# Optimization experiments

Measured on AMD Instinct MI355X. Metric: run time of the kernel, lower is better.

The kernel has to match this reference:

```python
import jax, jax.numpy as jnp
import numpy as np
import math

B, BERT_DIM, COND, INUM, RNN, TDIFF, SAMPLE_T, TEMB, TMAX = 16384, 768, 64, 10, 128, 200, 50, 64, 64


def _schedule():
    steps = TDIFF + 1
    x = np.linspace(0, TDIFF, steps) / TDIFF
    ab = np.cos((x + 0.008) / 1.008 * np.pi / 2) ** 2
    ab = ab / ab[0]
    betas = np.minimum(1.0 - ab[1:] / ab[:-1], 0.9999)
    alphas = 1.0 - betas
    alpha_bar = np.cumprod(alphas)
    stride = max(TDIFF // SAMPLE_T, 1)
    ts = np.array(list(range(TDIFF - 1, -1, -stride)), dtype=np.int64)  # 50 steps: 199..3
    abt = alpha_bar[ts]
    abp = np.where(ts > 0, alpha_bar[np.maximum(ts - 1, 0)], 1.0)
    beta = betas[ts]
    coef1 = np.sqrt(abp) * beta / (1 - abt)
    coef2 = np.sqrt(alphas[ts]) * (1 - abp) / (1 - abt)
    var = (1 - abp) / (1 - abt) * beta
    sqrtvar = np.where(ts > 0, np.sqrt(var), 0.0)
    return ts, coef1.astype(np.float32), coef2.astype(np.float32), sqrtvar.astype(np.float32)


def _sinusoidal_emb(ts, dim):
    half = dim // 2
    freq = jnp.exp(-math.log(10000.0) * jnp.arange(half, dtype=jnp.float32) / (half - 1))
    emb = ts.astype(jnp.float32)[:, None] * freq[None, :]
    return jnp.concatenate([jnp.sin(emb), jnp.cos(emb)], axis=-1)


def setup_inputs() -> dict:
    key = jax.random.key(0)
    ks = jax.random.split(key, 40)
    i = iter(range(40))

    def lin(kout, kin):  # torch Linear layout (out, in), Kaiming-ish scale
        kw, kb = jax.random.split(ks[next(i)])
        return (jax.random.normal(kw, (kout, kin), jnp.float32) / np.sqrt(kin),
                jax.random.normal(kb, (kout,), jnp.float32) * 0.01)

    inp = {}
    inp['bert_emb'] = jax.random.normal(ks[next(i)], (B, BERT_DIM), jnp.float32)
    # sorted, positive event times (padded)
    raw = jax.random.uniform(ks[next(i)], (B, TMAX), jnp.float32)
    inp['times'] = jnp.cumsum(raw * 0.05, axis=1)
    inp['init_noise'] = jax.random.normal(ks[next(i)], (B, INUM), jnp.float32)
    inp['step_noise'] = jax.random.normal(ks[next(i)], (SAMPLE_T, B, INUM), jnp.float32)

    inp['bp_w'], inp['bp_b'] = lin(COND, BERT_DIM)
    inp['ln_g'] = jnp.ones((COND,), jnp.float32)
    inp['ln_b'] = jnp.zeros((COND,), jnp.float32)
    inp['tp_w1'], inp['tp_b1'] = lin(TEMB * 2, TEMB)
    inp['tp_w2'], inp['tp_b2'] = lin(TEMB, TEMB * 2)
    den_in = INUM + COND + TEMB  # 138
    inp['dn_w1'], inp['dn_b1'] = lin(256, den_in)
    inp['dn_w2'], inp['dn_b2'] = lin(256, 256)
    inp['dn_w3'], inp['dn_b3'] = lin(INUM, 256)
    inp['sf_w1'], inp['sf_b1'] = lin(INUM * 2, INUM)
    inp['sf_w2'], inp['sf_b2'] = lin(INUM * 2, INUM * 2)
    inp['sf_w3'], inp['sf_b3'] = lin(INUM, INUM * 2)
    inp['h0_w'], inp['h0_b'] = lin(RNN, COND + INUM)
    inp['gru_wi'], inp['gru_bi'] = lin(3 * RNN, 1)
    inp['gru_wh'], inp['gru_bh'] = lin(3 * RNN, RNN)
    inp['hd_w'], inp['hd_b'] = lin(2, RNN)
    return inp


def _forward(bert_emb, times, init_noise, step_noise,
             bp_w, bp_b, ln_g, ln_b,
             tp_w1, tp_b1, tp_w2, tp_b2,
             dn_w1, dn_b1, dn_w2, dn_b2, dn_w3, dn_b3,
             sf_w1, sf_b1, sf_w2, sf_b2, sf_w3, sf_b3,
             h0_w, h0_b, gru_wi, gru_wh, gru_bi, gru_bh, hd_w, hd_b):
    # --- bert_proj: Linear + LayerNorm (dropout = identity at eval) ---
    c = bert_emb @ bp_w.T + bp_b
    mu = jnp.mean(c, axis=-1, keepdims=True)
    var = jnp.var(c, axis=-1, keepdims=True)
    cond = (c - mu) * jax.lax.rsqrt(var + 1e-5) * ln_g + ln_b  # (B, COND)

    # --- DDPM ancestral sampling over interval features ---
    ts_np, c1_np, c2_np, sv_np = _schedule()
    ts = jnp.asarray(ts_np)
    c1, c2, sv = jnp.asarray(c1_np), jnp.asarray(c2_np), jnp.asarray(sv_np)
    temb = _sinusoidal_emb(ts, TEMB)                     # (S, 64)
    te = jax.nn.silu(temb @ tp_w1.T + tp_b1) @ tp_w2.T + tp_b2  # (S, 64)

    def ddpm_step(x, args):
        te_s, c1_s, c2_s, sv_s, nz = args
        inp = jnp.concatenate([x, cond, jnp.broadcast_to(te_s, (x.shape[0], TEMB))], axis=-1)
        h = jax.nn.silu(inp @ dn_w1.T + dn_b1)
        h = jax.nn.silu(h @ dn_w2.T + dn_b2)
        x0p = h @ dn_w3.T + dn_b3
        x_new = c1_s * x0p + c2_s * x + sv_s * nz
        return x_new, None

    x0, _ = jax.lax.scan(ddpm_step, init_noise, (te, c1, c2, sv, step_noise))  # (B, INUM)

    # --- GRU decoder (teacher-forced forward_train) ---
    seq_emb = jax.nn.relu(x0 @ sf_w1.T + sf_b1)
    seq_emb = jax.nn.relu(seq_emb @ sf_w2.T + sf_b2)
    seq_emb = seq_emb @ sf_w3.T + sf_b3                  # (B, INUM)
    h0 = jnp.tanh(jnp.concatenate([cond, seq_emb], axis=-1) @ h0_w.T + h0_b)  # (B, RNN)

    gt_times = jnp.concatenate([jnp.zeros((times.shape[0], 1), times.dtype), times], axis=1)
    gt_delta = gt_times[:, 1:] - gt_times[:, :-1]        # (B, T)
    # x_in at step 0 is zeros, then gt_delta[:, i-1]
    x_in_seq = jnp.concatenate([jnp.zeros((1, times.shape[0], 1), times.dtype),
                                gt_delta.T[:, :, None]], axis=0)  # (T+1, B, 1)

    def gru_step(h, x_in):
        gi = x_in @ gru_wi.T + gru_bi                    # (B, 3*RNN)
        gh = h @ gru_wh.T + gru_bh
        gi_r, gi_z, gi_n = jnp.split(gi, 3, axis=-1)
        gh_r, gh_z, gh_n = jnp.split(gh, 3, axis=-1)
        r = jax.nn.sigmoid(gi_r + gh_r)
        z = jax.nn.sigmoid(gi_z + gh_z)
        n = jnp.tanh(gi_n + r * gh_n)
        h_new = (1.0 - z) * n + z * h
        out = h_new @ hd_w.T + hd_b                      # (B, 2)
        return h_new, out

    _, outs = jax.lax.scan(gru_step, h0, x_in_seq)       # (T+1, B, 2)
    pred_delta = outs[:, :, 0].T                         # (B, T+1)
    stop_logits = outs[:, :, 1].T
    return x0, pred_delta, stop_logits


def reference(bert_emb, times, init_noise, step_noise,
              bp_w, bp_b, ln_g, ln_b,
              tp_w1, tp_b1, tp_w2, tp_b2,
              dn_w1, dn_b1, dn_w2, dn_b2, dn_w3, dn_b3,
              sf_w1, sf_b1, sf_w2, sf_b2, sf_w3, sf_b3,
              h0_w, h0_b, gru_wi, gru_wh, gru_bi, gru_bh, hd_w, hd_b):
    return _forward(bert_emb, times, init_noise, step_noise,
                    bp_w, bp_b, ln_g, ln_b,
                    tp_w1, tp_b1, tp_w2, tp_b2,
                    dn_w1, dn_b1, dn_w2, dn_b2, dn_w3, dn_b3,
                    sf_w1, sf_b1, sf_w2, sf_b2, sf_w3, sf_b3,
                    h0_w, h0_b, gru_wi, gru_wh, gru_bi, gru_bh, hd_w, hd_b)
```

## Files before the change

### kernel.cpp

```cpp
#include <hip/hip_runtime.h>
#include <math.h>

typedef float f4 __attribute__((ext_vector_type(4)));
typedef float f32x4 __attribute__((ext_vector_type(4)));
typedef _Float16 f16;
typedef _Float16 f16x8 __attribute__((ext_vector_type(8)));

#define NB 16384
#define BERT_DIM 768
#define CONDD 64
#define INUMD 10
#define RNND 128
#define TDIFFN 200
#define SAMPLE_TN 50
#define TEMBD 64
#define TMAXN 64

struct Sched { float c1[SAMPLE_TN], c2[SAMPLE_TN], sv[SAMPLE_TN], ts[SAMPLE_TN]; };

__device__ __forceinline__ float fsig(float v)  { return __builtin_amdgcn_rcpf(1.f + __expf(-v)); }
__device__ __forceinline__ float ftanh(float v) { return 1.f - 2.f * __builtin_amdgcn_rcpf(1.f + __expf(2.f * v)); }
__device__ __forceinline__ float fsilu(float v) { return v * fsig(v); }

__global__ __launch_bounds__(256) void pack_kernel(
    const float* __restrict__ dn_w1, const float* __restrict__ dn_w2,
    const float* __restrict__ dn_w3, const float* __restrict__ gru_wh,
    const float* __restrict__ h0_w, const float* __restrict__ bp_w,
    float* __restrict__ w1ct, f16* __restrict__ w1x16, f16* __restrict__ w2f16,
    f16* __restrict__ whf16, float* __restrict__ h0wp, float* __restrict__ bp_wt,
    f16* __restrict__ w3f16)
{
    int idx = blockIdx.x * 256 + threadIdx.x;
    if (idx < 16384) { int k = idx >> 8, n = idx & 255; w1ct[idx] = dn_w1[n * 138 + 10 + k]; }
    if (idx < 8192)  { int n = idx >> 5, k = idx & 31; w1x16[idx] = (f16)(k < 10 ? dn_w1[n * 138 + k] : 0.f); }
    if (idx < 65536) { w2f16[idx] = (f16)dn_w2[idx]; }
    if (idx < 49152) { whf16[idx] = (f16)gru_wh[idx]; }
    if (idx < 9728)  { int r = idx / 76, c = idx % 76; h0wp[idx] = (c < 74) ? h0_w[r * 74 + c] : 0.f; }
    if (idx < 49152) { int k = idx / 64, n = idx % 64; bp_wt[idx] = bp_w[n * 768 + k]; }
    if (idx < 4096)  { int n = idx >> 8, k = idx & 255; w3f16[idx] = (f16)(n < 10 ? dn_w3[n * 256 + k] : 0.f); }
}

__global__ __launch_bounds__(512, 1) void bert2_kernel(
    const float* __restrict__ bert, const float* __restrict__ bp_wt,
    const float* __restrict__ bp_b, const float* __restrict__ ln_g,
    const float* __restrict__ ln_b, float* __restrict__ cond)
{
    __shared__ float At[64][68];
    __shared__ float outs[64][68];
    int tid = threadIdx.x;
    int row0 = blockIdx.x * 64;
    int cg = tid & 15, rg = tid >> 4;

    f4 acc[2];
    acc[0] = (f4)0.f; acc[1] = (f4)0.f;
    for (int p = 0; p < 12; ++p) {
        for (int u = tid; u < 64 * 16; u += 512) {
            int row = u >> 4, q = u & 15;
            *(f4*)(&At[row][q * 4]) = *(const f4*)(bert + (size_t)(row0 + row) * BERT_DIM + p * 64 + q * 4);
        }
        __syncthreads();
        for (int kq = 0; kq < 16; ++kq) {
            int k = p * 64 + kq * 4;
            f4 w0 = *(const f4*)(bp_wt + (size_t)(k + 0) * 64 + cg * 4);
            f4 w1 = *(const f4*)(bp_wt + (size_t)(k + 1) * 64 + cg * 4);
            f4 w2 = *(const f4*)(bp_wt + (size_t)(k + 2) * 64 + cg * 4);
            f4 w3 = *(const f4*)(bp_wt + (size_t)(k + 3) * 64 + cg * 4);
            #pragma unroll
            for (int i = 0; i < 2; ++i) {
                f4 a = *(const f4*)(&At[rg * 2 + i][kq * 4]);
                acc[i] += a[0] * w0 + a[1] * w1 + a[2] * w2 + a[3] * w3;
            }
        }
        __syncthreads();
    }
    f4 bb = *(const f4*)(bp_b + cg * 4);
    #pragma unroll
    for (int i = 0; i < 2; ++i) {
        f4 v = acc[i] + bb;
        *(f4*)(&outs[rg * 2 + i][cg * 4]) = v;
    }
    __syncthreads();
    {
        int row = tid >> 3, seg = tid & 7;
        f4 v0 = *(const f4*)(&outs[row][seg * 8]);
        f4 v1 = *(const f4*)(&outs[row][seg * 8 + 4]);
        float s = v0[0]+v0[1]+v0[2]+v0[3]+v1[0]+v1[1]+v1[2]+v1[3];
        float s2 = v0[0]*v0[0]+v0[1]*v0[1]+v0[2]*v0[2]+v0[3]*v0[3]
                 + v1[0]*v1[0]+v1[1]*v1[1]+v1[2]*v1[2]+v1[3]*v1[3];
        #pragma unroll
        for (int off = 1; off < 8; off <<= 1) { s += __shfl_xor(s, off); s2 += __shfl_xor(s2, off); }
        float mu = s * (1.f / 64.f);
        float var = s2 * (1.f / 64.f) - mu * mu;
        float inv = rsqrtf(var + 1e-5f);
        f4 g0 = *(const f4*)(ln_g + seg * 8), g1 = *(const f4*)(ln_g + seg * 8 + 4);
        f4 b0 = *(const f4*)(ln_b + seg * 8), b1 = *(const f4*)(ln_b + seg * 8 + 4);
        f4 o0, o1;
        #pragma unroll
        for (int j = 0; j < 4; ++j) {
            o0[j] = (v0[j] - mu) * inv * g0[j] + b0[j];
            o1[j] = (v1[j] - mu) * inv * g1[j] + b1[j];
        }
        float* dst = cond + (size_t)(row0 + row) * CONDD + seg * 8;
        *(f4*)dst = o0; *(f4*)(dst + 4) = o1;
    }
}

__global__ __launch_bounds__(128) void te_kernel(
    const float* __restrict__ tp_w1, const float* __restrict__ tp_b1,
    const float* __restrict__ tp_w2, const float* __restrict__ tp_b2,
    float* __restrict__ te, Sched sc)
{
    __shared__ float temb[TEMBD];
    __shared__ float h[TEMBD * 2];
    int s = blockIdx.x, t = threadIdx.x;
    if (t < 32) {
        float freq = expf(-logf(10000.f) * (float)t / 31.f);
        float e = sc.ts[s] * freq;
        temb[t] = sinf(e);
        temb[t + 32] = cosf(e);
    }
    __syncthreads();
    float a = tp_b1[t];
    for (int k = 0; k < TEMBD; ++k) a += temb[k] * tp_w1[t * TEMBD + k];
    h[t] = a * (1.f / (1.f + expf(-a)));
    __syncthreads();
    if (t < TEMBD) {
        float a2 = tp_b2[t];
        for (int k = 0; k < 128; ++k) a2 += h[k] * tp_w2[t * 128 + k];
        te[s * TEMBD + t] = a2;
    }
}

__global__ __launch_bounds__(256) void b1eff_kernel(
    const float* __restrict__ te, const float* __restrict__ dn_w1,
    const float* __restrict__ dn_b1, float* __restrict__ b1eff)
{
    __shared__ float tes[64];
    int s = blockIdx.x, n = threadIdx.x;
    if (n < 64) tes[n] = te[s * 64 + n];
    __syncthreads();
    float a = dn_b1[n];
    for (int k = 0; k < 64; ++k) a += tes[k] * dn_w1[n * 138 + 74 + k];
    b1eff[s * 256 + n] = a;
}

__global__ __launch_bounds__(256, 2) void ddpm_all_kernel(
    const float* __restrict__ x_init, const float* __restrict__ cond,
    const float* __restrict__ noise,
    const float* __restrict__ w1ct, const f16* __restrict__ w1x16,
    const float* __restrict__ b1eff, const f16* __restrict__ w2f16,
    const float* __restrict__ b2g, const f16* __restrict__ w3f16,
    const float* __restrict__ b3g, Sched sc, float* __restrict__ out_x0)
{
    __shared__ __align__(16) f16 h1[16 * 256];
    __shared__ __align__(16) f16 h2[16 * 256];
    __shared__ __align__(16) f16 xw[4][16 * 32];
    int tid = threadIdx.x;
    int row0 = blockIdx.x * 16;
    int lane = tid & 63, wn = tid >> 6;
    int l15 = lane & 15, l4 = lane >> 4;

    float* condl = (float*)h1;
    {
        int r = tid >> 4, q = tid & 15;
        *(f4*)(condl + r * 64 + q * 4) = *(const f4*)(cond + (size_t)(row0 + r) * 64 + q * 4);
    }
    *(f4*)((float*)&xw[wn][0] + lane * 4) = (f4)0.f;
    __syncthreads();

    f32x4 c1r[4];
    #pragma unroll
    for (int t = 0; t < 4; ++t) c1r[t] = (f32x4)0.f;
    for (int kq = 0; kq < 16; ++kq) {
        f4 cr[4];
        #pragma unroll
        for (int r = 0; r < 4; ++r) cr[r] = *(const f4*)(condl + (l4 * 4 + r) * 64 + kq * 4);
        #pragma unroll
        for (int t = 0; t < 4; ++t) {
            int col = wn * 64 + t * 16 + l15;
            #pragma unroll
            for (int j = 0; j < 4; ++j) {
                float w = w1ct[(kq * 4 + j) * 256 + col];
                #pragma unroll
                for (int r = 0; r < 4; ++r) c1r[t][r] += cr[r][j] * w;
            }
        }
    }
    __syncthreads();

    f16x8 B2[4][8], B1[4], W3[8];
    float b2v[4];
    #pragma unroll
    for (int t = 0; t < 4; ++t) {
        int col = wn * 64 + t * 16 + l15;
        B1[t] = *(const f16x8*)(w1x16 + col * 32 + l4 * 8);
        #pragma unroll
        for (int kb = 0; kb < 8; ++kb)
            B2[t][kb] = *(const f16x8*)(w2f16 + col * 256 + kb * 32 + l4 * 8);
        b2v[t] = b2g[col];
    }
    #pragma unroll
    for (int kb = 0; kb < 8; ++kb)
        W3[kb] = *(const f16x8*)(w3f16 + l15 * 256 + kb * 32 + l4 * 8);
    float b3v = (l15 < 10) ? b3g[l15] : 0.f;

    float xo[4] = {0.f, 0.f, 0.f, 0.f};
    if (l15 < 10) {
        #pragma unroll
        for (int r = 0; r < 4; ++r) {
            xo[r] = x_init[(size_t)(row0 + l4 * 4 + r) * INUMD + l15];
            xw[wn][(l4 * 4 + r) * 32 + l15] = (f16)xo[r];
        }
    }
    float be[4];
    #pragma unroll
    for (int t = 0; t < 4; ++t) be[t] = b1eff[wn * 64 + t * 16 + l15];

    int axoff = l15 * 64 + l4 * 16;
    #pragma unroll 1
    for (int s = 0; s < SAMPLE_TN; ++s) {
        f16x8 ax = *(const f16x8*)((const char*)xw[wn] + axoff);
        #pragma unroll
        for (int t = 0; t < 4; ++t) {
            f32x4 ci;
            #pragma unroll
            for (int r = 0; r < 4; ++r) ci[r] = c1r[t][r] + be[t];
            f32x4 a1 = __builtin_amdgcn_mfma_f32_16x16x32_f16(ax, B1[t], ci, 0, 0, 0);
            int col = wn * 64 + t * 16 + l15;
            #pragma unroll
            for (int r = 0; r < 4; ++r) {
                int row = l4 * 4 + r;
                *(f16*)((char*)h1 + ((row * 512 + col * 2) ^ ((row & 7) << 4))) = (f16)fsilu(a1[r]);
            }
        }
        float nz[4] = {0.f, 0.f, 0.f, 0.f};
        if (l15 < 10) {
            #pragma unroll
            for (int r = 0; r < 4; ++r)
                nz[r] = noise[((size_t)s * NB + row0 + l4 * 4 + r) * INUMD + l15];
        }
        if (s + 1 < SAMPLE_TN) {
            #pragma unroll
            for (int t = 0; t < 4; ++t) be[t] = b1eff[(s + 1) * 256 + wn * 64 + t * 16 + l15];
        }
        __syncthreads();
        {
            f32x4 a2[4];
            #pragma unroll
            for (int t = 0; t < 4; ++t) a2[t] = (f32x4)0.f;
            #pragma unroll
            for (int kb = 0; kb < 8; ++kb) {
                f16x8 A = *(const f16x8*)((const char*)h1 +
                          (l15 * 512 + ((kb * 64 + l4 * 16) ^ ((l15 & 7) << 4))));
                #pragma unroll
                for (int t = 0; t < 4; ++t)
                    a2[t] = __builtin_amdgcn_mfma_f32_16x16x32_f16(A, B2[t][kb], a2[t], 0, 0, 0);
            }
            #pragma unroll
            for (int t = 0; t < 4; ++t) {
                int col = wn * 64 + t * 16 + l15;
                #pragma unroll
                for (int r = 0; r < 4; ++r) {
                    int row = l4 * 4 + r;
                    *(f16*)((char*)h2 + ((row * 512 + col * 2) ^ ((row & 7) << 4))) = (f16)fsilu(a2[t][r] + b2v[t]);
                }
            }
        }
        __syncthreads();
        {
            f32x4 pa = (f32x4)0.f, pb = (f32x4)0.f;
            #pragma unroll
            for (int kb = 0; kb < 8; kb += 2) {
                f16x8 A0 = *(const f16x8*)((const char*)h2 +
                           (l15 * 512 + (((kb + 0) * 64 + l4 * 16) ^ ((l15 & 7) << 4))));
                f16x8 A1 = *(const f16x8*)((const char*)h2 +
                           (l15 * 512 + (((kb + 1) * 64 + l4 * 16) ^ ((l15 & 7) << 4))));
                pa = __builtin_amdgcn_mfma_f32_16x16x32_f16(A0, W3[kb + 0], pa, 0, 0, 0);
                pb = __builtin_amdgcn_mfma_f32_16x16x32_f16(A1, W3[kb + 1], pb, 0, 0, 0);
            }
            if (l15 < 10) {
                float c1s = sc.c1[s], c2s = sc.c2[s], svs = sc.sv[s];
                #pragma unroll
                for (int r = 0; r < 4; ++r) {
                    float xn = c1s * (pa[r] + pb[r] + b3v) + c2s * xo[r] + svs * nz[r];
                    xo[r] = xn;
                    xw[wn][(l4 * 4 + r) * 32 + l15] = (f16)xn;
                }
            }
        }
    }
    if (wn == 0 && l15 < 10) {
        #pragma unroll
        for (int r = 0; r < 4; ++r)
            out_x0[(size_t)(row0 + l4 * 4 + r) * INUMD + l15] = xo[r];
    }
}

__global__ __launch_bounds__(512, 4) void gru_all_kernel(
    const float* __restrict__ x0, const float* __restrict__ cond,
    const float* __restrict__ times,
    const float* __restrict__ sf_w1, const float* __restrict__ sf_b1,
    const float* __restrict__ sf_w2, const float* __restrict__ sf_b2,
    const float* __restrict__ sf_w3, const float* __restrict__ sf_b3,
    const float* __restrict__ h0wp, const float* __restrict__ h0_b,
    const f16* __restrict__ whf16, const float* __restrict__ gru_bh,
    const float* __restrict__ gru_wi, const float* __restrict__ gru_bi,
    const float* __restrict__ hd_w, const float* __restrict__ hd_b,
    float* __restrict__ pred, float* __restrict__ stopl)
{
    __shared__ __align__(16) f16 hl[2][32 * 128];
    __shared__ float dl[32 * 66];
    __shared__ __align__(16) float ubuf[4224];
    __shared__ __align__(16) f16 hds[2 * 128];
    __shared__ float wis[384], bis[384], bhs[384];
    int tid = threadIdx.x;
    int row0 = blockIdx.x * 32;
    int lane = tid & 63, wn = tid >> 6;
    int l15 = lane & 15, l4 = lane >> 4;

    if (tid < 384) { wis[tid] = gru_wi[tid]; bis[tid] = gru_bi[tid]; bhs[tid] = gru_bh[tid]; }
    if (tid < 256) hds[tid] = (f16)hd_w[tid];
    float* tb = ubuf;
    for (int u = tid; u < 2048; u += 512) {
        int r = u >> 6, k = u & 63;
        tb[u] = times[(size_t)(row0 + r) * TMAXN + k];
    }
    __syncthreads();
    float dtmp[5]; int c = 0;
    for (int idx = tid; idx < 2080; idx += 512) {
        int r = idx / 65, i = idx % 65;
        float v;
        if (i == 0) v = 0.f;
        else if (i == 1) v = tb[r * 64];
        else v = tb[r * 64 + i - 1] - tb[r * 64 + i - 2];
        dtmp[c++] = v;
    }
    __syncthreads();
    c = 0;
    for (int idx = tid; idx < 2080; idx += 512) {
        int r = idx / 65, i = idx % 65;
        dl[r * 66 + i] = dtmp[c++];
    }
    float* in2 = ubuf;
    float* sbuf = ubuf + 32 * 76;
    for (int idx = tid; idx < 2048; idx += 512) {
        int r = idx >> 6, k = idx & 63;
        in2[r * 76 + k] = cond[(size_t)(row0 + r) * CONDD + k];
    }
    for (int idx = tid; idx < 320; idx += 512) {
        int r = idx / 10, k = idx % 10;
        in2[r * 76 + 64 + k] = x0[(size_t)(row0 + r) * 10 + k];
    }
    if (tid < 64) { int r = tid >> 1; in2[r * 76 + 74 + (tid & 1)] = 0.f; }
    __syncthreads();
    for (int idx = tid; idx < 640; idx += 512) {
        int r = idx / 20, j = idx % 20;
        float a = sf_b1[j];
        for (int k = 0; k < 10; ++k) a += in2[r * 76 + 64 + k] * sf_w1[j * 10 + k];
        sbuf[r * 44 + j] = fmaxf(a, 0.f);
    }
    __syncthreads();
    for (int idx = tid; idx < 640; idx += 512) {
        int r = idx / 20, j = idx % 20;
        float a = sf_b2[j];
        for (int k = 0; k < 20; ++k) a += sbuf[r * 44 + k] * sf_w2[j * 20 + k];
        sbuf[r * 44 + 22 + j] = fmaxf(a, 0.f);
    }
    __syncthreads();
    for (int idx = tid; idx < 320; idx += 512) {
        int r = idx / 10, j = idx % 10;
        float a = sf_b3[j];
        for (int k = 0; k < 20; ++k) a += sbuf[r * 44 + 22 + k] * sf_w3[j * 20 + k];
        in2[r * 76 + 64 + j] = a;
    }
    __syncthreads();
    for (int idx = tid; idx < 4096; idx += 512) {
        int r = idx >> 7, j = idx & 127;
        float a = h0_b[j];
        const f4* wr = (const f4*)(h0wp + j * 76);
        const f4* iv = (const f4*)(in2 + r * 76);
        #pragma unroll
        for (int q = 0; q < 19; ++q) {
            f4 w = wr[q], v = iv[q];
            a += v[0] * w[0] + v[1] * w[1] + v[2] * w[2] + v[3] * w[3];
        }
        *(f16*)((char*)hl[0] + ((r * 256 + j * 2) ^ ((r & 7) << 4))) = (f16)ftanh(a);
    }
    __syncthreads();

    int jc = wn * 16 + l15;
    f16x8 BW[3][4];
    float wi_[3], bi_[3], bh_[3];
    #pragma unroll
    for (int g = 0; g < 3; ++g) {
        int col = g * 128 + jc;
        #pragma unroll
        for (int kb = 0; kb < 4; ++kb)
            BW[g][kb] = *(const f16x8*)(whf16 + col * 128 + kb * 32 + l4 * 8);
        wi_[g] = wis[col]; bi_[g] = bis[col]; bh_[g] = bhs[col];
    }
    float hb0 = hd_b[0], hb1 = hd_b[1];
    float hreg[2][4];
    #pragma unroll
    for (int mr = 0; mr < 2; ++mr)
        #pragma unroll
        for (int r = 0; r < 4; ++r) {
            int row = mr * 16 + l4 * 4 + r;
            hreg[mr][r] = (float)(*(const f16*)((const char*)hl[0] + ((row * 256 + jc * 2) ^ ((row & 7) << 4))));
        }
    float* outb = ubuf;

    #pragma unroll 1
    for (int s = 0; s < TMAXN + 1; ++s) {
        const f16* cur = hl[s & 1];
        f16* nxt = hl[(s + 1) & 1];
        #pragma unroll
        for (int mr = 0; mr < 2; ++mr) {
            int arow = mr * 16 + l15;
            int aswz = (arow & 7) << 4;
            f16x8 A[4];
            #pragma unroll
            for (int kb = 0; kb < 4; ++kb)
                A[kb] = *(const f16x8*)((const char*)cur + ((arow * 256 + kb * 64 + l4 * 16) ^ aswz));
            if (wn == 0 && s > 0) {
                float pa = 0.f, pb = 0.f;
                #pragma unroll
                for (int kb = 0; kb < 4; ++kb) {
                    f16x8 ha = *(const f16x8*)(hds + kb * 32 + l4 * 8);
                    f16x8 hbv = *(const f16x8*)(hds + 128 + kb * 32 + l4 * 8);
                    #pragma unroll
                    for (int e = 0; e < 8; ++e) {
                        pa += (float)(A[kb][e]) * (float)(ha[e]);
                        pb += (float)(A[kb][e]) * (float)(hbv[e]);
                    }
                }
                pa += __shfl_xor(pa, 16); pa += __shfl_xor(pa, 32);
                pb += __shfl_xor(pb, 16); pb += __shfl_xor(pb, 32);
                if (l4 == 0) {
                    outb[arow * 132 + (s - 1)] = pa + hb0;
                    outb[arow * 132 + 66 + (s - 1)] = pb + hb1;
                }
            }
            f32x4 acc[3];
            #pragma unroll
            for (int g = 0; g < 3; ++g) {
                f32x4 ci; ci[0] = ci[1] = ci[2] = ci[3] = bh_[g];
                acc[g] = ci;
            }
            #pragma unroll
            for (int kb = 0; kb < 4; ++kb)
                #pragma unroll
                for (int g = 0; g < 3; ++g)
                    acc[g] = __builtin_amdgcn_mfma_f32_16x16x32_f16(A[kb], BW[g][kb], acc[g], 0, 0, 0);
            #pragma unroll
            for (int r = 0; r < 4; ++r) {
                int row = mr * 16 + l4 * 4 + r;
                float xv = dl[row * 66 + s];
                float rr = fsig(xv * wi_[0] + bi_[0] + acc[0][r]);
                float zz = fsig(xv * wi_[1] + bi_[1] + acc[1][r]);
                float nn = ftanh(xv * wi_[2] + bi_[2] + rr * acc[2][r]);
                float hn = (1.f - zz) * nn + zz * hreg[mr][r];
                hreg[mr][r] = hn;
                *(f16*)((char*)nxt + ((row * 256 + jc * 2) ^ ((row & 7) << 4))) = (f16)hn;
            }
        }
        __syncthreads();
    }
    if (wn == 0) {
        #pragma unroll
        for (int mr = 0; mr < 2; ++mr) {
            int arow = mr * 16 + l15;
            int aswz = (arow & 7) << 4;
            float pa = 0.f, pb = 0.f;
            #pragma unroll
            for (int kb = 0; kb < 4; ++kb) {
                f16x8 A = *(const f16x8*)((const char*)hl[1] + ((arow * 256 + kb * 64 + l4 * 16) ^ aswz));
                f16x8 ha = *(const f16x8*)(hds + kb * 32 + l4 * 8);
                f16x8 hbv = *(const f16x8*)(hds + 128 + kb * 32 + l4 * 8);
                #pragma unroll
                for (int e = 0; e < 8; ++e) {
                    pa += (float)(A[e]) * (float)(ha[e]);
                    pb += (float)(A[e]) * (float)(hbv[e]);
                }
            }
            pa += __shfl_xor(pa, 16); pa += __shfl_xor(pa, 32);
            pb += __shfl_xor(pb, 16); pb += __shfl_xor(pb, 32);
            if (l4 == 0) {
                outb[arow * 132 + 64] = pa + hb0;
                outb[arow * 132 + 66 + 64] = pb + hb1;
            }
        }
    }
    __syncthreads();
    for (int u = tid; u < 2080; u += 512) {
        int r = u / 65, i = u % 65;
        pred[(size_t)(row0 + r) * (TMAXN + 1) + i] = outb[r * 132 + i];
        stopl[(size_t)(row0 + r) * (TMAXN + 1) + i] = outb[r * 132 + 66 + i];
    }
}

extern "C" void kernel_launch(void* const* d_in, const int* in_sizes, int n_in,
                              void* d_out, int out_size, void* d_ws, size_t ws_size,
                              hipStream_t stream)
{
    const float* bert       = (const float*)d_in[0];
    const float* times      = (const float*)d_in[1];
    const float* init_noise = (const float*)d_in[2];
    const float* step_noise = (const float*)d_in[3];
    const float* bp_w  = (const float*)d_in[4];
    const float* bp_b  = (const float*)d_in[5];
    const float* ln_g  = (const float*)d_in[6];
    const float* ln_b  = (const float*)d_in[7];
    const float* tp_w1 = (const float*)d_in[8];
    const float* tp_b1 = (const float*)d_in[9];
    const float* tp_w2 = (const float*)d_in[10];
    const float* tp_b2 = (const float*)d_in[11];
    const float* dn_w1 = (const float*)d_in[12];
    const float* dn_b1 = (const float*)d_in[13];
    const float* dn_w2 = (const float*)d_in[14];
    const float* dn_b2 = (const float*)d_in[15];
    const float* dn_w3 = (const float*)d_in[16];
    const float* dn_b3 = (const float*)d_in[17];
    const float* sf_w1 = (const float*)d_in[18];
    const float* sf_b1 = (const float*)d_in[19];
    const float* sf_w2 = (const float*)d_in[20];
    const float* sf_b2 = (const float*)d_in[21];
    const float* sf_w3 = (const float*)d_in[22];
    const float* sf_b3 = (const float*)d_in[23];
    const float* h0_w  = (const float*)d_in[24];
    const float* h0_b  = (const float*)d_in[25];
    const float* gru_wi = (const float*)d_in[26];
    const float* gru_bi = (const float*)d_in[27];
    const float* gru_wh = (const float*)d_in[28];
    const float* gru_bh = (const float*)d_in[29];
    const float* hd_w   = (const float*)d_in[30];
    const float* hd_b   = (const float*)d_in[31];

    float* ws    = (float*)d_ws;
    float* cond  = ws;
    float* te    = cond + (size_t)NB * CONDD;
    float* b1eff = te + SAMPLE_TN * TEMBD;
    float* w1ct  = b1eff + SAMPLE_TN * 256;
    float* h0wp  = w1ct + 64 * 256;
    float* bp_wt = h0wp + 128 * 76;
    f16*   w1x16 = (f16*)(bp_wt + 768 * 64);
    f16*   w2f16 = w1x16 + 256 * 32;
    f16*   whf16 = w2f16 + 256 * 256;
    f16*   w3f16 = whf16 + 384 * 128;

    double ab[TDIFFN + 1];
    for (int i = 0; i <= TDIFFN; ++i) {
        double xx = (double)i / (double)TDIFFN;
        double v = cos((xx + 0.008) / 1.008 * M_PI * 0.5);
        ab[i] = v * v;
    }
    double ab0 = ab[0];
    for (int i = 0; i <= TDIFFN; ++i) ab[i] /= ab0;
    double betas[TDIFFN], alphas[TDIFFN], abar[TDIFFN];
    double cp = 1.0;
    for (int i = 0; i < TDIFFN; ++i) {
        double b = 1.0 - ab[i + 1] / ab[i];
        if (b > 0.9999) b = 0.9999;
        betas[i] = b; alphas[i] = 1.0 - b;
        cp *= alphas[i]; abar[i] = cp;
    }
    Sched sc;
    for (int s = 0; s < SAMPLE_TN; ++s) {
        int tt = TDIFFN - 1 - 4 * s;
        double abt = abar[tt];
        double abp = (tt > 0) ? abar[tt - 1] : 1.0;
        double beta = betas[tt];
        sc.c1[s] = (float)(sqrt(abp) * beta / (1.0 - abt));
        sc.c2[s] = (float)(sqrt(alphas[tt]) * (1.0 - abp) / (1.0 - abt));
        sc.sv[s] = (float)((tt > 0) ? sqrt((1.0 - abp) / (1.0 - abt) * beta) : 0.0);
        sc.ts[s] = (float)tt;
    }

    float* out    = (float*)d_out;
    float* out_x0 = out;
    float* pred   = out + (size_t)NB * INUMD;
    float* stopl  = pred + (size_t)NB * (TMAXN + 1);

    pack_kernel<<<256, 256, 0, stream>>>(dn_w1, dn_w2, dn_w3, gru_wh, h0_w, bp_w,
                                         w1ct, w1x16, w2f16, whf16, h0wp, bp_wt, w3f16);
    bert2_kernel<<<NB / 64, 512, 0, stream>>>(bert, bp_wt, bp_b, ln_g, ln_b, cond);
    te_kernel<<<SAMPLE_TN, 128, 0, stream>>>(tp_w1, tp_b1, tp_w2, tp_b2, te, sc);
    b1eff_kernel<<<SAMPLE_TN, 256, 0, stream>>>(te, dn_w1, dn_b1, b1eff);

    ddpm_all_kernel<<<NB / 16, 256, 0, stream>>>(
        init_noise, cond, step_noise, w1ct, w1x16, b1eff, w2f16, dn_b2, w3f16, dn_b3,
        sc, out_x0);

    gru_all_kernel<<<NB / 32, 512, 0, stream>>>(
        out_x0, cond, times,
        sf_w1, sf_b1, sf_w2, sf_b2, sf_w3, sf_b3,
        h0wp, h0_b, whf16, gru_bh, gru_wi, gru_bi, hd_w, hd_b,
        pred, stopl);
}
```

Before: 571.0 us.

## Use MFMA for bert projection and double rows per block in DDPM kernel

Rewrites the bert projection plus layernorm kernel as an fp16 MFMA GEMM. It stages the whole converted weight matrix in swizzled LDS and does the layernorm reduction in registers. The DDPM sampling kernel now handles 32 rows per block instead of 16, so the register-resident W1/W2 fragments are reused over twice the rows, and W3 moves from registers into LDS. The changes trade fp16 rounding of the bert inputs and higher register/LDS pressure for fewer blocks and less scalar FMA work.

```diff
diff --git a/kernel.cpp b/kernel.cpp
--- a/kernel.cpp
+++ b/kernel.cpp
@@ -27,7 +27,7 @@
     const float* __restrict__ dn_w3, const float* __restrict__ gru_wh,
     const float* __restrict__ h0_w, const float* __restrict__ bp_w,
     float* __restrict__ w1ct, f16* __restrict__ w1x16, f16* __restrict__ w2f16,
-    f16* __restrict__ whf16, float* __restrict__ h0wp, float* __restrict__ bp_wt,
+    f16* __restrict__ whf16, float* __restrict__ h0wp, f16* __restrict__ bpw16,
     f16* __restrict__ w3f16)
 {
     int idx = blockIdx.x * 256 + threadIdx.x;
@@ -36,72 +36,79 @@
     if (idx < 65536) { w2f16[idx] = (f16)dn_w2[idx]; }
     if (idx < 49152) { whf16[idx] = (f16)gru_wh[idx]; }
     if (idx < 9728)  { int r = idx / 76, c = idx % 76; h0wp[idx] = (c < 74) ? h0_w[r * 74 + c] : 0.f; }
-    if (idx < 49152) { int k = idx / 64, n = idx % 64; bp_wt[idx] = bp_w[n * 768 + k]; }
+    if (idx < 49152) { bpw16[idx] = (f16)bp_w[idx]; }
     if (idx < 4096)  { int n = idx >> 8, k = idx & 255; w3f16[idx] = (f16)(n < 10 ? dn_w3[n * 256 + k] : 0.f); }
 }
 
-__global__ __launch_bounds__(512, 1) void bert2_kernel(
-    const float* __restrict__ bert, const float* __restrict__ bp_wt,
+__global__ __launch_bounds__(256, 1) void bert2_kernel(
+    const float* __restrict__ bert, const f16* __restrict__ bpw16,
     const float* __restrict__ bp_b, const float* __restrict__ ln_g,
     const float* __restrict__ ln_b, float* __restrict__ cond)
 {
-    __shared__ float At[64][68];
-    __shared__ float outs[64][68];
+    __shared__ __align__(16) f16 ws16[64 * 768];
     int tid = threadIdx.x;
     int row0 = blockIdx.x * 64;
-    int cg = tid & 15, rg = tid >> 4;
-
-    f4 acc[2];
-    acc[0] = (f4)0.f; acc[1] = (f4)0.f;
-    for (int p = 0; p < 12; ++p) {
-        for (int u = tid; u < 64 * 16; u += 512) {
-            int row = u >> 4, q = u & 15;
-            *(f4*)(&At[row][q * 4]) = *(const f4*)(bert + (size_t)(row0 + row) * BERT_DIM + p * 64 + q * 4);
-        }
-        __syncthreads();
-        for (int kq = 0; kq < 16; ++kq) {
-            int k = p * 64 + kq * 4;
-            f4 w0 = *(const f4*)(bp_wt + (size_t)(k + 0) * 64 + cg * 4);
-            f4 w1 = *(const f4*)(bp_wt + (size_t)(k + 1) * 64 + cg * 4);
-            f4 w2 = *(const f4*)(bp_wt + (size_t)(k + 2) * 64 + cg * 4);
-            f4 w3 = *(const f4*)(bp_wt + (size_t)(k + 3) * 64 + cg * 4);
-            #pragma unroll
-            for (int i = 0; i < 2; ++i) {
-                f4 a = *(const f4*)(&At[rg * 2 + i][kq * 4]);
-                acc[i] += a[0] * w0 + a[1] * w1 + a[2] * w2 + a[3] * w3;
-            }
-        }
-        __syncthreads();
-    }
-    f4 bb = *(const f4*)(bp_b + cg * 4);
-    #pragma unroll
-    for (int i = 0; i < 2; ++i) {
-        f4 v = acc[i] + bb;
-        *(f4*)(&outs[rg * 2 + i][cg * 4]) = v;
-    }
-    __syncthreads();
-    {
-        int row = tid >> 3, seg = tid & 7;
-        f4 v0 = *(const f4*)(&outs[row][seg * 8]);
-        f4 v1 = *(const f4*)(&outs[row][seg * 8 + 4]);
-        float s = v0[0]+v0[1]+v0[2]+v0[3]+v1[0]+v1[1]+v1[2]+v1[3];
-        float s2 = v0[0]*v0[0]+v0[1]*v0[1]+v0[2]*v0[2]+v0[3]*v0[3]
-                 + v1[0]*v1[0]+v1[1]*v1[1]+v1[2]*v1[2]+v1[3]*v1[3];
-        #pragma unroll
-        for (int off = 1; off < 8; off <<= 1) { s += __shfl_xor(s, off); s2 += __shfl_xor(s2, off); }
-        float mu = s * (1.f / 64.f);
-        float var = s2 * (1.f / 64.f) - mu * mu;
-        float inv = rsqrtf(var + 1e-5f);
-        f4 g0 = *(const f4*)(ln_g + seg * 8), g1 = *(const f4*)(ln_g + seg * 8 + 4);
-        f4 b0 = *(const f4*)(ln_b + seg * 8), b1 = *(const f4*)(ln_b + seg * 8 + 4);
-        f4 o0, o1;
-        #pragma unroll
-        for (int j = 0; j < 4; ++j) {
-            o0[j] = (v0[j] - mu) * inv * g0[j] + b0[j];
-            o1[j] = (v1[j] - mu) * inv * g1[j] + b1[j];
-        }
-        float* dst = cond + (size_t)(row0 + row) * CONDD + seg * 8;
-        *(f4*)dst = o0; *(f4*)(dst + 4) = o1;
+    int lane = tid & 63, wn = tid >> 6;
+    int l15 = lane & 15, l4 = lane >> 4;
+
+    for (int u = tid; u < 6144; u += 256) {
+        int n = u / 96, k8 = u % 96;
+        *(f16x8*)((char*)ws16 + n * 1536 + ((k8 * 16) ^ ((n & 7) << 4))) =
+            *(const f16x8*)(bpw16 + n * 768 + k8 * 8);
+    }
+    __syncthreads();
+
+    const float* aptr = bert + (size_t)(row0 + wn * 16 + l15) * BERT_DIM;
+    f32x4 acc[4];
+    #pragma unroll
+    for (int t = 0; t < 4; ++t) {
+        float bb = bp_b[t * 16 + l15];
+        acc[t][0] = bb; acc[t][1] = bb; acc[t][2] = bb; acc[t][3] = bb;
+    }
+    #pragma unroll 4
+    for (int kb = 0; kb < 24; ++kb) {
+        f4 a0 = *(const f4*)(aptr + kb * 32 + l4 * 8);
+        f4 a1 = *(const f4*)(aptr + kb * 32 + l4 * 8 + 4);
+        f16x8 af;
+        #pragma unroll
+        for (int j = 0; j < 4; ++j) { af[j] = (f16)a0[j]; af[4 + j] = (f16)a1[j]; }
+        #pragma unroll
+        for (int t = 0; t < 4; ++t) {
+            int col = t * 16 + l15;
+            f16x8 bf = *(const f16x8*)((const char*)ws16 +
+                        (col * 1536 + ((kb * 64 + l4 * 16) ^ ((col & 7) << 4))));
+            acc[t] = __builtin_amdgcn_mfma_f32_16x16x32_f16(af, bf, acc[t], 0, 0, 0);
+        }
+    }
+    float s[4] = {0,0,0,0}, s2[4] = {0,0,0,0};
+    #pragma unroll
+    for (int r = 0; r < 4; ++r)
+        #pragma unroll
+        for (int t = 0; t < 4; ++t) { float v = acc[t][r]; s[r] += v; s2[r] += v * v; }
+    #pragma unroll
+    for (int r = 0; r < 4; ++r) {
+        #pragma unroll
+        for (int off = 1; off < 16; off <<= 1) {
+            s[r] += __shfl_xor(s[r], off);
+            s2[r] += __shfl_xor(s2[r], off);
+        }
+    }
+    float mu[4], inv[4];
+    #pragma unroll
+    for (int r = 0; r < 4; ++r) {
+        mu[r] = s[r] * (1.f / 64.f);
+        float var = s2[r] * (1.f / 64.f) - mu[r] * mu[r];
+        inv[r] = rsqrtf(var + 1e-5f);
+    }
+    #pragma unroll
+    for (int t = 0; t < 4; ++t) {
+        int col = t * 16 + l15;
+        float g = ln_g[col], b = ln_b[col];
+        #pragma unroll
+        for (int r = 0; r < 4; ++r) {
+            int row = row0 + wn * 16 + l4 * 4 + r;
+            cond[(size_t)row * CONDD + col] = (acc[t][r] - mu[r]) * inv[r] * g + b;
+        }
     }
 }
 
@@ -152,29 +159,40 @@
     const float* __restrict__ b2g, const f16* __restrict__ w3f16,
     const float* __restrict__ b3g, Sched sc, float* __restrict__ out_x0)
 {
-    __shared__ __align__(16) f16 h1[16 * 256];
-    __shared__ __align__(16) f16 h2[16 * 256];
-    __shared__ __align__(16) f16 xw[4][16 * 32];
+    __shared__ __align__(16) f16 h1[32 * 256];
+    __shared__ __align__(16) f16 h2[32 * 256];
+    __shared__ __align__(16) f16 xw[4][32 * 32];
+    __shared__ __align__(16) f16 w3s[16 * 256];
     int tid = threadIdx.x;
-    int row0 = blockIdx.x * 16;
+    int row0 = blockIdx.x * 32;
     int lane = tid & 63, wn = tid >> 6;
     int l15 = lane & 15, l4 = lane >> 4;
 
     float* condl = (float*)h1;
-    {
-        int r = tid >> 4, q = tid & 15;
+    for (int u = tid; u < 32 * 16; u += 256) {
+        int r = u >> 4, q = u & 15;
         *(f4*)(condl + r * 64 + q * 4) = *(const f4*)(cond + (size_t)(row0 + r) * 64 + q * 4);
     }
+    for (int u = tid; u < 4096; u += 256) {
+        int n = u >> 8, k = u & 255;
+        *(f16*)((char*)w3s + (n * 512 + ((k * 2) ^ ((n & 7) << 4)))) = w3f16[u];
+    }
     *(f4*)((float*)&xw[wn][0] + lane * 4) = (f4)0.f;
-    __syncthreads();
-
-    f32x4 c1r[4];
-    #pragma unroll
-    for (int t = 0; t < 4; ++t) c1r[t] = (f32x4)0.f;
+    *(f4*)((float*)&xw[wn][0] + 256 + lane * 4) = (f4)0.f;
+    __syncthreads();
+
+    f32x4 c1r[2][4];
+    #pragma unroll
+    for (int mg = 0; mg < 2; ++mg)
+        #pragma unroll
+        for (int t = 0; t < 4; ++t) c1r[mg][t] = (f32x4)0.f;
     for (int kq = 0; kq < 16; ++kq) {
-        f4 cr[4];
-        #pragma unroll
-        for (int r = 0; r < 4; ++r) cr[r] = *(const f4*)(condl + (l4 * 4 + r) * 64 + kq * 4);
+        f4 cr0[4], cr1[4];
+        #pragma unroll
+        for (int r = 0; r < 4; ++r) {
+            cr0[r] = *(const f4*)(condl + (l4 * 4 + r) * 64 + kq * 4);
+            cr1[r] = *(const f4*)(condl + (16 + l4 * 4 + r) * 64 + kq * 4);
+        }
         #pragma unroll
         for (int t = 0; t < 4; ++t) {
             int col = wn * 64 + t * 16 + l15;
@@ -182,13 +200,16 @@
             for (int j = 0; j < 4; ++j) {
                 float w = w1ct[(kq * 4 + j) * 256 + col];
                 #pragma unroll
-                for (int r = 0; r < 4; ++r) c1r[t][r] += cr[r][j] * w;
-            }
-        }
-    }
-    __syncthreads();
-
-    f16x8 B2[4][8], B1[4], W3[8];
+                for (int r = 0; r < 4; ++r) {
+                    c1r[0][t][r] += cr0[r][j] * w;
+                    c1r[1][t][r] += cr1[r][j] * w;
+                }
+            }
+        }
+    }
+    __syncthreads();
+
+    f16x8 B2[4][8], B1[4];
     float b2v[4];
     #pragma unroll
     for (int t = 0; t < 4; ++t) {
@@ -199,59 +220,65 @@
             B2[t][kb] = *(const f16x8*)(w2f16 + col * 256 + kb * 32 + l4 * 8);
         b2v[t] = b2g[col];
     }
-    #pragma unroll
-    for (int kb = 0; kb < 8; ++kb)
-        W3[kb] = *(const f16x8*)(w3f16 + l15 * 256 + kb * 32 + l4 * 8);
     float b3v = (l15 < 10) ? b3g[l15] : 0.f;
 
-    float xo[4] = {0.f, 0.f, 0.f, 0.f};
+    float xo[2][4] = {{0.f,0.f,0.f,0.f},{0.f,0.f,0.f,0.f}};
     if (l15 < 10) {
         #pragma unroll
-        for (int r = 0; r < 4; ++r) {
-            xo[r] = x_init[(size_t)(row0 + l4 * 4 + r) * INUMD + l15];
-            xw[wn][(l4 * 4 + r) * 32 + l15] = (f16)xo[r];
-        }
+        for (int mg = 0; mg < 2; ++mg)
+            #pragma unroll
+            for (int r = 0; r < 4; ++r) {
+                int row = mg * 16 + l4 * 4 + r;
+                xo[mg][r] = x_init[(size_t)(row0 + row) * INUMD + l15];
+                xw[wn][row * 32 + l15] = (f16)xo[mg][r];
+            }
     }
     float be[4];
     #pragma unroll
     for (int t = 0; t < 4; ++t) be[t] = b1eff[wn * 64 + t * 16 + l15];
 
-    int axoff = l15 * 64 + l4 * 16;
     #pragma unroll 1
     for (int s = 0; s < SAMPLE_TN; ++s) {
-        f16x8 ax = *(const f16x8*)((const char*)xw[wn] + axoff);
-        #pragma unroll
-        for (int t = 0; t < 4; ++t) {
-            f32x4 ci;
-            #pragma unroll
-            for (int r = 0; r < 4; ++r) ci[r] = c1r[t][r] + be[t];
-            f32x4 a1 = __builtin_amdgcn_mfma_f32_16x16x32_f16(ax, B1[t], ci, 0, 0, 0);
-            int col = wn * 64 + t * 16 + l15;
-            #pragma unroll
-            for (int r = 0; r < 4; ++r) {
-                int row = l4 * 4 + r;
-                *(f16*)((char*)h1 + ((row * 512 + col * 2) ^ ((row & 7) << 4))) = (f16)fsilu(a1[r]);
-            }
-        }
-        float nz[4] = {0.f, 0.f, 0.f, 0.f};
+        #pragma unroll
+        for (int mg = 0; mg < 2; ++mg) {
+            f16x8 ax = *(const f16x8*)((const char*)&xw[wn][0] + mg * 1024 + l15 * 64 + l4 * 16);
+            #pragma unroll
+            for (int t = 0; t < 4; ++t) {
+                f32x4 ci;
+                #pragma unroll
+                for (int r = 0; r < 4; ++r) ci[r] = c1r[mg][t][r] + be[t];
+                f32x4 a1 = __builtin_amdgcn_mfma_f32_16x16x32_f16(ax, B1[t], ci, 0, 0, 0);
+                int col = wn * 64 + t * 16 + l15;
+                #pragma unroll
+                for (int r = 0; r < 4; ++r) {
+                    int row = mg * 16 + l4 * 4 + r;
+                    *(f16*)((char*)h1 + ((row * 512 + col * 2) ^ ((row & 7) << 4))) = (f16)fsilu(a1[r]);
+                }
+            }
+        }
+        float nz[2][4] = {{0.f,0.f,0.f,0.f},{0.f,0.f,0.f,0.f}};
         if (l15 < 10) {
             #pragma unroll
-            for (int r = 0; r < 4; ++r)
-                nz[r] = noise[((size_t)s * NB + row0 + l4 * 4 + r) * INUMD + l15];
+            for (int mg = 0; mg < 2; ++mg)
+                #pragma unroll
+                for (int r = 0; r < 4; ++r)
+                    nz[mg][r] = noise[((size_t)s * NB + row0 + mg * 16 + l4 * 4 + r) * INUMD + l15];
         }
         if (s + 1 < SAMPLE_TN) {
             #pragma unroll
             for (int t = 0; t < 4; ++t) be[t] = b1eff[(s + 1) * 256 + wn * 64 + t * 16 + l15];
         }
         __syncthreads();
-        {
+        #pragma unroll
+        for (int mg = 0; mg < 2; ++mg) {
+            int arow = mg * 16 + l15;
             f32x4 a2[4];
             #pragma unroll
             for (int t = 0; t < 4; ++t) a2[t] = (f32x4)0.f;
             #pragma unroll
             for (int kb = 0; kb < 8; ++kb) {
                 f16x8 A = *(const f16x8*)((const char*)h1 +
-                          (l15 * 512 + ((kb * 64 + l4 * 16) ^ ((l15 & 7) << 4))));
+                          (arow * 512 + ((kb * 64 + l4 * 16) ^ ((arow & 7) << 4))));
                 #pragma unroll
                 for (int t = 0; t < 4; ++t)
                     a2[t] = __builtin_amdgcn_mfma_f32_16x16x32_f16(A, B2[t][kb], a2[t], 0, 0, 0);
@@ -261,38 +288,45 @@
                 int col = wn * 64 + t * 16 + l15;
                 #pragma unroll
                 for (int r = 0; r < 4; ++r) {
-                    int row = l4 * 4 + r;
+                    int row = mg * 16 + l4 * 4 + r;
                     *(f16*)((char*)h2 + ((row * 512 + col * 2) ^ ((row & 7) << 4))) = (f16)fsilu(a2[t][r] + b2v[t]);
                 }
             }
         }
         __syncthreads();
-        {
+        #pragma unroll
+        for (int mg = 0; mg < 2; ++mg) {
+            int arow = mg * 16 + l15;
             f32x4 pa = (f32x4)0.f, pb = (f32x4)0.f;
             #pragma unroll
             for (int kb = 0; kb < 8; kb += 2) {
-                f16x8 A0 = *(const f16x8*)((const char*)h2 +
-                           (l15 * 512 + (((kb + 0) * 64 + l4 * 16) ^ ((l15 & 7) << 4))));
-                f16x8 A1 = *(const f16x8*)((const char*)h2 +
-                           (l15 * 512 + (((kb + 1) * 64 + l4 * 16) ^ ((l15 & 7) << 4))));
-                pa = __builtin_amdgcn_mfma_f32_16x16x32_f16(A0, W3[kb + 0], pa, 0, 0, 0);
-                pb = __builtin_amdgcn_mfma_f32_16x16x32_f16(A1, W3[kb + 1], pb, 0, 0, 0);
+                int off0 = ((kb + 0) * 64 + l4 * 16) ^ ((l15 & 7) << 4);
+                int off1 = ((kb + 1) * 64 + l4 * 16) ^ ((l15 & 7) << 4);
+                f16x8 A0 = *(const f16x8*)((const char*)h2 + (arow * 512 + off0));
+                f16x8 W0 = *(const f16x8*)((const char*)w3s + (l15 * 512 + off0));
+                f16x8 A1 = *(const f16x8*)((const char*)h2 + (arow * 512 + off1));
+                f16x8 W1 = *(const f16x8*)((const char*)w3s + (l15 * 512 + off1));
+                pa = __builtin_amdgcn_mfma_f32_16x16x32_f16(A0, W0, pa, 0, 0, 0);
+                pb = __builtin_amdgcn_mfma_f32_16x16x32_f16(A1, W1, pb, 0, 0, 0);
             }
             if (l15 < 10) {
                 float c1s = sc.c1[s], c2s = sc.c2[s], svs = sc.sv[s];
                 #pragma unroll
                 for (int r = 0; r < 4; ++r) {
-                    float xn = c1s * (pa[r] + pb[r] + b3v) + c2s * xo[r] + svs * nz[r];
-                    xo[r] = xn;
-                    xw[wn][(l4 * 4 + r) * 32 + l15] = (f16)xn;
+                    int row = mg * 16 + l4 * 4 + r;
+                    float xn = c1s * (pa[r] + pb[r] + b3v) + c2s * xo[mg][r] + svs * nz[mg][r];
+                    xo[mg][r] = xn;
+                    xw[wn][row * 32 + l15] = (f16)xn;
                 }
             }
         }
     }
     if (wn == 0 && l15 < 10) {
         #pragma unroll
-        for (int r = 0; r < 4; ++r)
-            out_x0[(size_t)(row0 + l4 * 4 + r) * INUMD + l15] = xo[r];
+        for (int mg = 0; mg < 2; ++mg)
+            #pragma unroll
+            for (int r = 0; r < 4; ++r)
+                out_x0[(size_t)(row0 + mg * 16 + l4 * 4 + r) * INUMD + l15] = xo[mg][r];
     }
 }
 
@@ -542,11 +576,11 @@
     float* b1eff = te + SAMPLE_TN * TEMBD;
     float* w1ct  = b1eff + SAMPLE_TN * 256;
     float* h0wp  = w1ct + 64 * 256;
-    float* bp_wt = h0wp + 128 * 76;
-    f16*   w1x16 = (f16*)(bp_wt + 768 * 64);
+    f16*   w1x16 = (f16*)(h0wp + 128 * 76);
     f16*   w2f16 = w1x16 + 256 * 32;
     f16*   whf16 = w2f16 + 256 * 256;
     f16*   w3f16 = whf16 + 384 * 128;
+    f16*   bpw16 = w3f16 + 16 * 256;
 
     double ab[TDIFFN + 1];
     for (int i = 0; i <= TDIFFN; ++i) {
@@ -582,12 +616,12 @@
     float* stopl  = pred + (size_t)NB * (TMAXN + 1);
 
     pack_kernel<<<256, 256, 0, stream>>>(dn_w1, dn_w2, dn_w3, gru_wh, h0_w, bp_w,
-                                         w1ct, w1x16, w2f16, whf16, h0wp, bp_wt, w3f16);
-    bert2_kernel<<<NB / 64, 512, 0, stream>>>(bert, bp_wt, bp_b, ln_g, ln_b, cond);
+                                         w1ct, w1x16, w2f16, whf16, h0wp, bpw16, w3f16);
+    bert2_kernel<<<NB / 64, 256, 0, stream>>>(bert, bpw16, bp_b, ln_g, ln_b, cond);
     te_kernel<<<SAMPLE_TN, 128, 0, stream>>>(tp_w1, tp_b1, tp_w2, tp_b2, te, sc);
     b1eff_kernel<<<SAMPLE_TN, 256, 0, stream>>>(te, dn_w1, dn_b1, b1eff);
 
-    ddpm_all_kernel<<<NB / 16, 256, 0, stream>>>(
+    ddpm_all_kernel<<<NB / 32, 256, 0, stream>>>(
         init_noise, cond, step_noise, w1ct, w1x16, b1eff, w2f16, dn_b2, w3f16, dn_b3,
         sc, out_x0);
 
```

New measurement: 1.079 ms. +88.9%, slower.
